# Kernel optimization log

Measured on AMD Instinct MI355X. Metric: run time of the kernel, lower is better.

Reference implementation:

```python
import jax, jax.numpy as jnp
import numpy as np

NUM_USERS = 100000
NUM_ITEMS = 200000
D = 128          # embedding_dim
K = 4            # num interest heads
B = 4096
H = 256          # history length
H1, H2 = 512, 256  # hidden_units


def setup_inputs() -> dict:
    key = jax.random.key(0)
    ks = jax.random.split(key, 10)
    inp = {
        "user_ids": jax.random.randint(ks[0], (B,), 0, NUM_USERS),
        "candidate_items": jax.random.randint(ks[1], (B,), 0, NUM_ITEMS),
        "history_items": jax.random.randint(ks[2], (B, H), 0, NUM_ITEMS),
        "item_table": jax.random.normal(ks[3], (NUM_ITEMS, D), dtype=jnp.float32) * 0.05,
        "Wp": jax.random.normal(ks[4], (D, K), dtype=jnp.float32) * (1.0 / np.sqrt(D)),
        "W1": jax.random.normal(ks[5], (2 * D, H1), dtype=jnp.float32) * (1.0 / np.sqrt(2 * D)),
        "b1": jnp.zeros((H1,), dtype=jnp.float32),
        "W2": jax.random.normal(ks[6], (H1, H2), dtype=jnp.float32) * (1.0 / np.sqrt(H1)),
        "b2": jnp.zeros((H2,), dtype=jnp.float32),
        "W3": jax.random.normal(ks[7], (H2, 1), dtype=jnp.float32) * (1.0 / np.sqrt(H2)),
        "b3": jnp.zeros((1,), dtype=jnp.float32),
    }
    return inp


def reference(user_ids, candidate_items, history_items, item_table, Wp,
              W1, b1, W2, b2, W3, b3):
    # user_ids is unused by the original forward (user_emb never applied)
    item_vecs = item_table[history_items]          # (B, H, D)
    cand_vec = item_table[candidate_items]         # (B, D)

    # per-interest attention scores, softmax over history axis
    scores = jnp.einsum('bhd,dk->bhk', item_vecs, Wp)   # (B, H, K)
    scores = jax.nn.softmax(scores, axis=1)

    # softmax-weighted pooling -> K interest vectors per user
    interest_vectors = jnp.einsum('bhk,bhd->bkd', scores, item_vecs)  # (B, K, D)

    # similarity to candidate, pick best interest (data-dependent gather)
    sim_scores = jnp.einsum('bkd,bd->bk', interest_vectors, cand_vec)  # (B, K)
    best_idx = jnp.argmax(sim_scores, axis=-1)                          # (B,)
    selected = jnp.take_along_axis(
        interest_vectors, best_idx[:, None, None], axis=1)[:, 0, :]    # (B, D)

    # MLP tail: [2D -> 512] ReLU [512 -> 256] ReLU [256 -> 1], sigmoid
    x = jnp.concatenate([selected, cand_vec], axis=-1)  # (B, 2D)
    x = jax.nn.relu(x @ W1 + b1)
    x = jax.nn.relu(x @ W2 + b2)
    out = (x @ W3 + b3)[:, 0]                            # (B,)
    return jax.nn.sigmoid(out)
```

## Files before the change

### kernel.cpp

```cpp
#include <hip/hip_runtime.h>
#include <hip/hip_bf16.h>
#include <math.h>

#define B_SZ   4096
#define H_LEN  256
#define D_DIM  128
#define K_HEADS 4
#define H1_DIM 512
#define H2_DIM 256

#define CH     64
#define NCH    4
#define TPAD   132
#define H1PAD  520

typedef __attribute__((ext_vector_type(8))) short bf16x8;
typedef __attribute__((ext_vector_type(4))) float f32x4;

__global__ __launch_bounds__(256, 4) void interest_kernel(
    const int*   __restrict__ cand_ids,
    const int*   __restrict__ hist,
    const float* __restrict__ table,
    const float* __restrict__ Wp,
    const float* __restrict__ W1,
    const float* __restrict__ W2,
    __hip_bfloat16* __restrict__ W1t,
    __hip_bfloat16* __restrict__ W2t,
    __hip_bfloat16* __restrict__ Xbf)
{
    if (blockIdx.x >= B_SZ) {
        int idx = (blockIdx.x - B_SZ) * 256 + threadIdx.x;
        if (idx < 2 * D_DIM * H1_DIM) {
            int n = idx >> 8, k = idx & 255;
            W1t[idx] = __float2bfloat16(W1[k * H1_DIM + n]);
        } else {
            int j = idx - 2 * D_DIM * H1_DIM;
            int n = j >> 9, k = j & 511;
            W2t[j] = __float2bfloat16(W2[k * H2_DIM + n]);
        }
        return;
    }

    __shared__ float tile[CH * TPAD];
    __shared__ float wpt[K_HEADS * D_DIM];
    __shared__ float exps4[CH * 4];
    __shared__ float candv[D_DIM];
    __shared__ int   rowids[H_LEN];
    __shared__ float lsumW[16];
    __shared__ float simred[4][K_HEADS];
    __shared__ int   bestk;

    const int b    = blockIdx.x;
    const int t    = threadIdx.x;
    const int lane = t & 63, w = t >> 6;
    const int r    = t >> 2, q = t & 3;
    const int d    = t & 127, half = t >> 7;

    if (t < D_DIM) {
        float4 w4 = ((const float4*)Wp)[t];
        wpt[0 * D_DIM + t] = w4.x;
        wpt[1 * D_DIM + t] = w4.y;
        wpt[2 * D_DIM + t] = w4.z;
        wpt[3 * D_DIM + t] = w4.w;
    }
    const int cand = cand_ids[b];
    if (t >= 128 && t < 160) {
        int c = t - 128;
        ((float4*)candv)[c] = ((const float4*)(table + (long long)cand * D_DIM))[c];
    }
    rowids[t] = hist[(long long)b * H_LEN + t];

    float a0 = 0.f, a1 = 0.f, a2 = 0.f, a3 = 0.f;
    float l0 = 0.f, l1 = 0.f, l2 = 0.f, l3 = 0.f;

    for (int c = 0; c < NCH; ++c) {
        __syncthreads();

        const int   row = rowids[(c << 6) + r];
        const float* rp = table + (long long)row * D_DIM + (q << 2);
        float4 v0 = *(const float4*)(rp + 0 * 16);
        float4 v1 = *(const float4*)(rp + 1 * 16);
        float4 v2 = *(const float4*)(rp + 2 * 16);
        float4 v3 = *(const float4*)(rp + 3 * 16);
        float4 v4 = *(const float4*)(rp + 4 * 16);
        float4 v5 = *(const float4*)(rp + 5 * 16);
        float4 v6 = *(const float4*)(rp + 6 * 16);
        float4 v7 = *(const float4*)(rp + 7 * 16);

        float s0 = 0.f, s1 = 0.f, s2 = 0.f, s3 = 0.f;
        float4 va;
        #define DO_J(J, VV)                                                     \
        {   va = VV;                                                            \
            const int cb = (q << 2) + (J << 4);                                 \
            float4 w0 = *(const float4*)(wpt + 0 * D_DIM + cb);                 \
            float4 w1 = *(const float4*)(wpt + 1 * D_DIM + cb);                 \
            float4 w2 = *(const float4*)(wpt + 2 * D_DIM + cb);                 \
            float4 w3 = *(const float4*)(wpt + 3 * D_DIM + cb);                 \
            s0 += va.x * w0.x + va.y * w0.y + va.z * w0.z + va.w * w0.w;        \
            s1 += va.x * w1.x + va.y * w1.y + va.z * w1.z + va.w * w1.w;        \
            s2 += va.x * w2.x + va.y * w2.y + va.z * w2.z + va.w * w2.w;        \
            s3 += va.x * w3.x + va.y * w3.y + va.z * w3.z + va.w * w3.w;        \
            *(float4*)(tile + r * TPAD + cb) = va;                              \
        }
        DO_J(0, v0) DO_J(1, v1) DO_J(2, v2) DO_J(3, v3)
        DO_J(4, v4) DO_J(5, v5) DO_J(6, v6) DO_J(7, v7)
        #undef DO_J

        s0 += __shfl_xor(s0, 1); s0 += __shfl_xor(s0, 2);
        s1 += __shfl_xor(s1, 1); s1 += __shfl_xor(s1, 2);
        s2 += __shfl_xor(s2, 1); s2 += __shfl_xor(s2, 2);
        s3 += __shfl_xor(s3, 1); s3 += __shfl_xor(s3, 2);

        float e0 = expf(s0), e1 = expf(s1), e2 = expf(s2), e3 = expf(s3);
        if (q == 0) ((float4*)exps4)[r] = make_float4(e0, e1, e2, e3);

        float t0 = e0, t1 = e1, t2 = e2, t3 = e3;
        #pragma unroll
        for (int off = 4; off <= 32; off <<= 1) {
            t0 += __shfl_xor(t0, off);
            t1 += __shfl_xor(t1, off);
            t2 += __shfl_xor(t2, off);
            t3 += __shfl_xor(t3, off);
        }
        l0 += t0; l1 += t1; l2 += t2; l3 += t3;

        __syncthreads();

        #pragma unroll 8
        for (int i = 0; i < 32; ++i) {
            int hl = (half << 5) + i;
            float4 e4 = ((const float4*)exps4)[hl];
            float  vv = tile[hl * TPAD + d];
            a0 += e4.x * vv; a1 += e4.y * vv; a2 += e4.z * vv; a3 += e4.w * vv;
        }
    }

    __syncthreads();
    float* partBp = tile;
    float* ivbufp = tile + 512;

    if (half == 1) ((float4*)partBp)[d] = make_float4(a0, a1, a2, a3);
    if (lane == 0) ((float4*)lsumW)[w]  = make_float4(l0, l1, l2, l3);
    __syncthreads();

    float s0 = 0.f, s1 = 0.f, s2 = 0.f, s3 = 0.f;
    if (half == 0) {
        float4 pb = ((const float4*)partBp)[d];
        float4 L0 = ((const float4*)lsumW)[0];
        float4 L1 = ((const float4*)lsumW)[1];
        float4 L2 = ((const float4*)lsumW)[2];
        float4 L3 = ((const float4*)lsumW)[3];
        float i0 = 1.f / (L0.x + L1.x + L2.x + L3.x);
        float i1 = 1.f / (L0.y + L1.y + L2.y + L3.y);
        float i2 = 1.f / (L0.z + L1.z + L2.z + L3.z);
        float i3 = 1.f / (L0.w + L1.w + L2.w + L3.w);
        a0 = (a0 + pb.x) * i0;
        a1 = (a1 + pb.y) * i1;
        a2 = (a2 + pb.z) * i2;
        a3 = (a3 + pb.w) * i3;
        ((float4*)ivbufp)[d] = make_float4(a0, a1, a2, a3);
        float cd = candv[d];
        s0 = a0 * cd; s1 = a1 * cd; s2 = a2 * cd; s3 = a3 * cd;
    }
    #pragma unroll
    for (int off = 32; off >= 1; off >>= 1) {
        s0 += __shfl_xor(s0, off);
        s1 += __shfl_xor(s1, off);
        s2 += __shfl_xor(s2, off);
        s3 += __shfl_xor(s3, off);
    }
    if (lane == 0) {
        simred[w][0] = s0; simred[w][1] = s1;
        simred[w][2] = s2; simred[w][3] = s3;
    }
    __syncthreads();

    if (t == 0) {
        float sim[4];
        #pragma unroll
        for (int k = 0; k < 4; ++k)
            sim[k] = simred[0][k] + simred[1][k] + simred[2][k] + simred[3][k];
        int best = 0;
        #pragma unroll
        for (int k = 1; k < 4; ++k) if (sim[k] > sim[best]) best = k;
        bestk = best;
    }
    __syncthreads();

    __hip_bfloat16* xrow = Xbf + (long long)b * (2 * D_DIM);
    if (t < 128) xrow[t] = __float2bfloat16(ivbufp[t * 4 + bestk]);
    else         xrow[t] = __float2bfloat16(candv[t - 128]);
}

__global__ __launch_bounds__(256) void fused_mlp(
    const __hip_bfloat16* __restrict__ Xbf,
    const __hip_bfloat16* __restrict__ W1t,
    const float* __restrict__ b1,
    const __hip_bfloat16* __restrict__ W2t,
    const float* __restrict__ b2,
    const float* __restrict__ W3,
    const float* __restrict__ b3,
    float* __restrict__ out)
{
    __shared__ __hip_bfloat16 H1s[64 * H1PAD];

    const int t    = threadIdx.x;
    const int wave = t >> 6, lane = t & 63;
    const int lm   = lane & 15, quad = lane >> 4;
    const int mrow = blockIdx.x * 64 + wave * 16;
    const int lrow = wave * 16;

    const __hip_bfloat16* Ap = Xbf + (long long)(mrow + lm) * 256 + quad * 8;
    bf16x8 afr[8];
    #pragma unroll
    for (int j = 0; j < 8; ++j) afr[j] = *(const bf16x8*)(Ap + j * 32);

    #pragma unroll 4
    for (int nt = 0; nt < 32; ++nt) {
        const int n = nt * 16 + lm;
        const __hip_bfloat16* Bp = W1t + (long long)n * 256 + quad * 8;
        f32x4 acc = {0.f, 0.f, 0.f, 0.f};
        #pragma unroll
        for (int j = 0; j < 8; ++j) {
            bf16x8 bfr = *(const bf16x8*)(Bp + j * 32);
            acc = __builtin_amdgcn_mfma_f32_16x16x32_bf16(afr[j], bfr, acc, 0, 0, 0);
        }
        const float bv = b1[n];
        #pragma unroll
        for (int i = 0; i < 4; ++i) {
            float v = fmaxf(acc[i] + bv, 0.f);
            H1s[(lrow + quad * 4 + i) * H1PAD + n] = __float2bfloat16(v);
        }
    }

    bf16x8 hfr[16];
    #pragma unroll
    for (int j = 0; j < 16; ++j)
        hfr[j] = *(const bf16x8*)(&H1s[(lrow + lm) * H1PAD + j * 32 + quad * 8]);

    float hp[4] = {0.f, 0.f, 0.f, 0.f};
    #pragma unroll 2
    for (int nt = 0; nt < 16; ++nt) {
        const int n = nt * 16 + lm;
        const __hip_bfloat16* Bp = W2t + (long long)n * 512 + quad * 8;
        f32x4 acc = {0.f, 0.f, 0.f, 0.f};
        #pragma unroll
        for (int j = 0; j < 16; ++j) {
            bf16x8 bfr = *(const bf16x8*)(Bp + j * 32);
            acc = __builtin_amdgcn_mfma_f32_16x16x32_bf16(hfr[j], bfr, acc, 0, 0, 0);
        }
        const float bv = b2[n], w3v = W3[n];
        #pragma unroll
        for (int i = 0; i < 4; ++i)
            hp[i] += fmaxf(acc[i] + bv, 0.f) * w3v;
    }

    #pragma unroll
    for (int off = 1; off <= 8; off <<= 1) {
        hp[0] += __shfl_xor(hp[0], off);
        hp[1] += __shfl_xor(hp[1], off);
        hp[2] += __shfl_xor(hp[2], off);
        hp[3] += __shfl_xor(hp[3], off);
    }
    if (lm == 0) {
        const float bb = b3[0];
        #pragma unroll
        for (int i = 0; i < 4; ++i) {
            float z = hp[i] + bb;
            out[mrow + quad * 4 + i] = 1.f / (1.f + expf(-z));
        }
    }
}

extern "C" void kernel_launch(void* const* d_in, const int* in_sizes, int n_in,
                              void* d_out, int out_size, void* d_ws, size_t ws_size,
                              hipStream_t stream) {
    const int*   cand  = (const int*)  d_in[1];
    const int*   hist  = (const int*)  d_in[2];
    const float* table = (const float*)d_in[3];
    const float* Wp    = (const float*)d_in[4];
    const float* W1    = (const float*)d_in[5];
    const float* b1    = (const float*)d_in[6];
    const float* W2    = (const float*)d_in[7];
    const float* b2    = (const float*)d_in[8];
    const float* W3    = (const float*)d_in[9];
    const float* b3    = (const float*)d_in[10];
    float* out = (float*)d_out;

    char* p = (char*)d_ws;
    __hip_bfloat16* Xbf = (__hip_bfloat16*)p;  p += (size_t)B_SZ * 2 * D_DIM * 2;
    __hip_bfloat16* W1t = (__hip_bfloat16*)p;  p += (size_t)H1_DIM * 2 * D_DIM * 2;
    __hip_bfloat16* W2t = (__hip_bfloat16*)p;

    interest_kernel<<<B_SZ + 1024, 256, 0, stream>>>(
        cand, hist, table, Wp, W1, W2, W1t, W2t, Xbf);
    fused_mlp<<<B_SZ / 64, 256, 0, stream>>>(Xbf, W1t, b1, W2t, b2, W3, b3, out);
}
```

Measured before the change: 297.1 us.

## Gather history embeddings from a per-call fp16 copy of the item table

When the workspace is large enough, a new kernel converts the whole fp32 item table to fp16 on every call. The interest kernel then gathers history rows at half the bytes, processing 128 rows per chunk with two threads per row and an fp16 shared tile. This targets the bandwidth cost of the random-row gather, but adds a full-table read and write each call and lowers precision. The launch-bounds occupancy hint drops from 4 to 2, and the old fp32 kernel is kept as a fallback when the workspace is too small.

```diff
diff --git a/kernel.cpp b/kernel.cpp
--- a/kernel.cpp
+++ b/kernel.cpp
@@ -8,42 +8,68 @@
 #define K_HEADS 4
 #define H1_DIM 512
 #define H2_DIM 256
+#define NUM_ITEMS 200000
 
 #define CH     64
 #define NCH    4
 #define TPAD   132
 #define H1PAD  520
 
+#define CH2    128
+#define NCH2   2
+#define TP2    136
+
 typedef __attribute__((ext_vector_type(8))) short bf16x8;
 typedef __attribute__((ext_vector_type(4))) float f32x4;
-
-__global__ __launch_bounds__(256, 4) void interest_kernel(
+typedef _Float16 fp16x8 __attribute__((ext_vector_type(8)));
+
+__global__ __launch_bounds__(256) void convert_table(
+    const float* __restrict__ table, _Float16* __restrict__ t16)
+{
+    const int tid = blockIdx.x * 256 + threadIdx.x;
+    float4 a = ((const float4*)table)[tid * 2];
+    float4 b = ((const float4*)table)[tid * 2 + 1];
+    fp16x8 h;
+    h[0] = (_Float16)a.x; h[1] = (_Float16)a.y;
+    h[2] = (_Float16)a.z; h[3] = (_Float16)a.w;
+    h[4] = (_Float16)b.x; h[5] = (_Float16)b.y;
+    h[6] = (_Float16)b.z; h[7] = (_Float16)b.w;
+    ((fp16x8*)t16)[tid] = h;
+}
+
+__device__ __forceinline__ void weight_convert_block(
+    int blk, int t, const float* W1, const float* W2,
+    __hip_bfloat16* W1t, __hip_bfloat16* W2t)
+{
+    int idx = blk * 256 + t;
+    if (idx < 2 * D_DIM * H1_DIM) {
+        int n = idx >> 8, k = idx & 255;
+        W1t[idx] = __float2bfloat16(W1[k * H1_DIM + n]);
+    } else {
+        int j = idx - 2 * D_DIM * H1_DIM;
+        int n = j >> 9, k = j & 511;
+        W2t[j] = __float2bfloat16(W2[k * H2_DIM + n]);
+    }
+}
+
+__global__ __launch_bounds__(256, 2) void interest_kernel_f16(
     const int*   __restrict__ cand_ids,
     const int*   __restrict__ hist,
     const float* __restrict__ table,
+    const _Float16* __restrict__ t16,
     const float* __restrict__ Wp,
-    const float* __restrict__ W1,
-    const float* __restrict__ W2,
-    __hip_bfloat16* __restrict__ W1t,
-    __hip_bfloat16* __restrict__ W2t,
+    const float* __restrict__ W1, const float* __restrict__ W2,
+    __hip_bfloat16* __restrict__ W1t, __hip_bfloat16* __restrict__ W2t,
     __hip_bfloat16* __restrict__ Xbf)
 {
     if (blockIdx.x >= B_SZ) {
-        int idx = (blockIdx.x - B_SZ) * 256 + threadIdx.x;
-        if (idx < 2 * D_DIM * H1_DIM) {
-            int n = idx >> 8, k = idx & 255;
-            W1t[idx] = __float2bfloat16(W1[k * H1_DIM + n]);
-        } else {
-            int j = idx - 2 * D_DIM * H1_DIM;
-            int n = j >> 9, k = j & 511;
-            W2t[j] = __float2bfloat16(W2[k * H2_DIM + n]);
-        }
+        weight_convert_block(blockIdx.x - B_SZ, threadIdx.x, W1, W2, W1t, W2t);
         return;
     }
 
-    __shared__ float tile[CH * TPAD];
+    __shared__ __align__(16) _Float16 tile_h[CH2 * TP2];
     __shared__ float wpt[K_HEADS * D_DIM];
-    __shared__ float exps4[CH * 4];
+    __shared__ float exps4[CH2 * 4];
     __shared__ float candv[D_DIM];
     __shared__ int   rowids[H_LEN];
     __shared__ float lsumW[16];
@@ -53,7 +79,7 @@
     const int b    = blockIdx.x;
     const int t    = threadIdx.x;
     const int lane = t & 63, w = t >> 6;
-    const int r    = t >> 2, q = t & 3;
+    const int rr   = t >> 1, q = t & 1;
     const int d    = t & 127, half = t >> 7;
 
     if (t < D_DIM) {
@@ -73,50 +99,55 @@
     float a0 = 0.f, a1 = 0.f, a2 = 0.f, a3 = 0.f;
     float l0 = 0.f, l1 = 0.f, l2 = 0.f, l3 = 0.f;
 
-    for (int c = 0; c < NCH; ++c) {
+    for (int c = 0; c < NCH2; ++c) {
         __syncthreads();
 
-        const int   row = rowids[(c << 6) + r];
-        const float* rp = table + (long long)row * D_DIM + (q << 2);
-        float4 v0 = *(const float4*)(rp + 0 * 16);
-        float4 v1 = *(const float4*)(rp + 1 * 16);
-        float4 v2 = *(const float4*)(rp + 2 * 16);
-        float4 v3 = *(const float4*)(rp + 3 * 16);
-        float4 v4 = *(const float4*)(rp + 4 * 16);
-        float4 v5 = *(const float4*)(rp + 5 * 16);
-        float4 v6 = *(const float4*)(rp + 6 * 16);
-        float4 v7 = *(const float4*)(rp + 7 * 16);
+        const int row = rowids[(c << 7) + rr];
+        const fp16x8* rp = (const fp16x8*)(t16 + (long long)row * D_DIM + (q << 6));
+        fp16x8 v0 = rp[0], v1 = rp[1], v2 = rp[2], v3 = rp[3];
+        fp16x8 v4 = rp[4], v5 = rp[5], v6 = rp[6], v7 = rp[7];
 
         float s0 = 0.f, s1 = 0.f, s2 = 0.f, s3 = 0.f;
-        float4 va;
         #define DO_J(J, VV)                                                     \
-        {   va = VV;                                                            \
-            const int cb = (q << 2) + (J << 4);                                 \
-            float4 w0 = *(const float4*)(wpt + 0 * D_DIM + cb);                 \
-            float4 w1 = *(const float4*)(wpt + 1 * D_DIM + cb);                 \
-            float4 w2 = *(const float4*)(wpt + 2 * D_DIM + cb);                 \
-            float4 w3 = *(const float4*)(wpt + 3 * D_DIM + cb);                 \
-            s0 += va.x * w0.x + va.y * w0.y + va.z * w0.z + va.w * w0.w;        \
-            s1 += va.x * w1.x + va.y * w1.y + va.z * w1.z + va.w * w1.w;        \
-            s2 += va.x * w2.x + va.y * w2.y + va.z * w2.z + va.w * w2.w;        \
-            s3 += va.x * w3.x + va.y * w3.y + va.z * w3.z + va.w * w3.w;        \
-            *(float4*)(tile + r * TPAD + cb) = va;                              \
+        {   fp16x8 va = VV;                                                     \
+            const int db = (q << 6) + (J << 3);                                 \
+            float ax = (float)va[0], ay = (float)va[1];                         \
+            float az = (float)va[2], aw = (float)va[3];                         \
+            float bx = (float)va[4], by = (float)va[5];                         \
+            float bz = (float)va[6], bw = (float)va[7];                         \
+            float4 w0l = *(const float4*)(wpt + 0 * D_DIM + db);                \
+            float4 w0h = *(const float4*)(wpt + 0 * D_DIM + db + 4);            \
+            float4 w1l = *(const float4*)(wpt + 1 * D_DIM + db);                \
+            float4 w1h = *(const float4*)(wpt + 1 * D_DIM + db + 4);            \
+            float4 w2l = *(const float4*)(wpt + 2 * D_DIM + db);                \
+            float4 w2h = *(const float4*)(wpt + 2 * D_DIM + db + 4);            \
+            float4 w3l = *(const float4*)(wpt + 3 * D_DIM + db);                \
+            float4 w3h = *(const float4*)(wpt + 3 * D_DIM + db + 4);            \
+            s0 += ax*w0l.x + ay*w0l.y + az*w0l.z + aw*w0l.w                     \
+                + bx*w0h.x + by*w0h.y + bz*w0h.z + bw*w0h.w;                    \
+            s1 += ax*w1l.x + ay*w1l.y + az*w1l.z + aw*w1l.w                     \
+                + bx*w1h.x + by*w1h.y + bz*w1h.z + bw*w1h.w;                    \
+            s2 += ax*w2l.x + ay*w2l.y + az*w2l.z + aw*w2l.w                     \
+                + bx*w2h.x + by*w2h.y + bz*w2h.z + bw*w2h.w;                    \
+            s3 += ax*w3l.x + ay*w3l.y + az*w3l.z + aw*w3l.w                     \
+                + bx*w3h.x + by*w3h.y + bz*w3h.z + bw*w3h.w;                    \
+            *(fp16x8*)(tile_h + rr * TP2 + db) = va;                            \
         }
         DO_J(0, v0) DO_J(1, v1) DO_J(2, v2) DO_J(3, v3)
         DO_J(4, v4) DO_J(5, v5) DO_J(6, v6) DO_J(7, v7)
         #undef DO_J
 
-        s0 += __shfl_xor(s0, 1); s0 += __shfl_xor(s0, 2);
-        s1 += __shfl_xor(s1, 1); s1 += __shfl_xor(s1, 2);
-        s2 += __shfl_xor(s2, 1); s2 += __shfl_xor(s2, 2);
-        s3 += __shfl_xor(s3, 1); s3 += __shfl_xor(s3, 2);
+        s0 += __shfl_xor(s0, 1);
+        s1 += __shfl_xor(s1, 1);
+        s2 += __shfl_xor(s2, 1);
+        s3 += __shfl_xor(s3, 1);
 
         float e0 = expf(s0), e1 = expf(s1), e2 = expf(s2), e3 = expf(s3);
-        if (q == 0) ((float4*)exps4)[r] = make_float4(e0, e1, e2, e3);
+        if (q == 0) ((float4*)exps4)[rr] = make_float4(e0, e1, e2, e3);
 
         float t0 = e0, t1 = e1, t2 = e2, t3 = e3;
         #pragma unroll
-        for (int off = 4; off <= 32; off <<= 1) {
+        for (int off = 2; off <= 32; off <<= 1) {
             t0 += __shfl_xor(t0, off);
             t1 += __shfl_xor(t1, off);
             t2 += __shfl_xor(t2, off);
@@ -127,17 +158,17 @@
         __syncthreads();
 
         #pragma unroll 8
-        for (int i = 0; i < 32; ++i) {
-            int hl = (half << 5) + i;
+        for (int i = 0; i < 64; ++i) {
+            int hl = (half << 6) + i;
             float4 e4 = ((const float4*)exps4)[hl];
-            float  vv = tile[hl * TPAD + d];
+            float  vv = (float)tile_h[hl * TP2 + d];
             a0 += e4.x * vv; a1 += e4.y * vv; a2 += e4.z * vv; a3 += e4.w * vv;
         }
     }
 
     __syncthreads();
-    float* partBp = tile;
-    float* ivbufp = tile + 512;
+    float* partBp = (float*)tile_h;
+    float* ivbufp = (float*)tile_h + 512;
 
     if (half == 1) ((float4*)partBp)[d] = make_float4(a0, a1, a2, a3);
     if (lane == 0) ((float4*)lsumW)[w]  = make_float4(l0, l1, l2, l3);
@@ -192,6 +223,171 @@
     else         xrow[t] = __float2bfloat16(candv[t - 128]);
 }
 
+__global__ __launch_bounds__(256, 4) void interest_kernel_f32(
+    const int*   __restrict__ cand_ids,
+    const int*   __restrict__ hist,
+    const float* __restrict__ table,
+    const float* __restrict__ Wp,
+    const float* __restrict__ W1, const float* __restrict__ W2,
+    __hip_bfloat16* __restrict__ W1t, __hip_bfloat16* __restrict__ W2t,
+    __hip_bfloat16* __restrict__ Xbf)
+{
+    if (blockIdx.x >= B_SZ) {
+        weight_convert_block(blockIdx.x - B_SZ, threadIdx.x, W1, W2, W1t, W2t);
+        return;
+    }
+
+    __shared__ float tile[CH * TPAD];
+    __shared__ float wpt[K_HEADS * D_DIM];
+    __shared__ float exps4[CH * 4];
+    __shared__ float candv[D_DIM];
+    __shared__ int   rowids[H_LEN];
+    __shared__ float lsumW[16];
+    __shared__ float simred[4][K_HEADS];
+    __shared__ int   bestk;
+
+    const int b    = blockIdx.x;
+    const int t    = threadIdx.x;
+    const int lane = t & 63, w = t >> 6;
+    const int r    = t >> 2, q = t & 3;
+    const int d    = t & 127, half = t >> 7;
+
+    if (t < D_DIM) {
+        float4 w4 = ((const float4*)Wp)[t];
+        wpt[0 * D_DIM + t] = w4.x;
+        wpt[1 * D_DIM + t] = w4.y;
+        wpt[2 * D_DIM + t] = w4.z;
+        wpt[3 * D_DIM + t] = w4.w;
+    }
+    const int cand = cand_ids[b];
+    if (t >= 128 && t < 160) {
+        int c = t - 128;
+        ((float4*)candv)[c] = ((const float4*)(table + (long long)cand * D_DIM))[c];
+    }
+    rowids[t] = hist[(long long)b * H_LEN + t];
+
+    float a0 = 0.f, a1 = 0.f, a2 = 0.f, a3 = 0.f;
+    float l0 = 0.f, l1 = 0.f, l2 = 0.f, l3 = 0.f;
+
+    for (int c = 0; c < NCH; ++c) {
+        __syncthreads();
+
+        const int   row = rowids[(c << 6) + r];
+        const float* rp = table + (long long)row * D_DIM + (q << 2);
+        float4 v0 = *(const float4*)(rp + 0 * 16);
+        float4 v1 = *(const float4*)(rp + 1 * 16);
+        float4 v2 = *(const float4*)(rp + 2 * 16);
+        float4 v3 = *(const float4*)(rp + 3 * 16);
+        float4 v4 = *(const float4*)(rp + 4 * 16);
+        float4 v5 = *(const float4*)(rp + 5 * 16);
+        float4 v6 = *(const float4*)(rp + 6 * 16);
+        float4 v7 = *(const float4*)(rp + 7 * 16);
+
+        float s0 = 0.f, s1 = 0.f, s2 = 0.f, s3 = 0.f;
+        float4 va;
+        #define DO_J(J, VV)                                                     \
+        {   va = VV;                                                            \
+            const int cb = (q << 2) + (J << 4);                                 \
+            float4 w0 = *(const float4*)(wpt + 0 * D_DIM + cb);                 \
+            float4 w1 = *(const float4*)(wpt + 1 * D_DIM + cb);                 \
+            float4 w2 = *(const float4*)(wpt + 2 * D_DIM + cb);                 \
+            float4 w3 = *(const float4*)(wpt + 3 * D_DIM + cb);                 \
+            s0 += va.x * w0.x + va.y * w0.y + va.z * w0.z + va.w * w0.w;        \
+            s1 += va.x * w1.x + va.y * w1.y + va.z * w1.z + va.w * w1.w;        \
+            s2 += va.x * w2.x + va.y * w2.y + va.z * w2.z + va.w * w2.w;        \
+            s3 += va.x * w3.x + va.y * w3.y + va.z * w3.z + va.w * w3.w;        \
+            *(float4*)(tile + r * TPAD + cb) = va;                              \
+        }
+        DO_J(0, v0) DO_J(1, v1) DO_J(2, v2) DO_J(3, v3)
+        DO_J(4, v4) DO_J(5, v5) DO_J(6, v6) DO_J(7, v7)
+        #undef DO_J
+
+        s0 += __shfl_xor(s0, 1); s0 += __shfl_xor(s0, 2);
+        s1 += __shfl_xor(s1, 1); s1 += __shfl_xor(s1, 2);
+        s2 += __shfl_xor(s2, 1); s2 += __shfl_xor(s2, 2);
+        s3 += __shfl_xor(s3, 1); s3 += __shfl_xor(s3, 2);
+
+        float e0 = expf(s0), e1 = expf(s1), e2 = expf(s2), e3 = expf(s3);
+        if (q == 0) ((float4*)exps4)[r] = make_float4(e0, e1, e2, e3);
+
+        float t0 = e0, t1 = e1, t2 = e2, t3 = e3;
+        #pragma unroll
+        for (int off = 4; off <= 32; off <<= 1) {
+            t0 += __shfl_xor(t0, off);
+            t1 += __shfl_xor(t1, off);
+            t2 += __shfl_xor(t2, off);
+            t3 += __shfl_xor(t3, off);
+        }
+        l0 += t0; l1 += t1; l2 += t2; l3 += t3;
+
+        __syncthreads();
+
+        #pragma unroll 8
+        for (int i = 0; i < 32; ++i) {
+            int hl = (half << 5) + i;
+            float4 e4 = ((const float4*)exps4)[hl];
+            float  vv = tile[hl * TPAD + d];
+            a0 += e4.x * vv; a1 += e4.y * vv; a2 += e4.z * vv; a3 += e4.w * vv;
+        }
+    }
+
+    __syncthreads();
+    float* partBp = tile;
+    float* ivbufp = tile + 512;
+
+    if (half == 1) ((float4*)partBp)[d] = make_float4(a0, a1, a2, a3);
+    if (lane == 0) ((float4*)lsumW)[w]  = make_float4(l0, l1, l2, l3);
+    __syncthreads();
+
+    float s0 = 0.f, s1 = 0.f, s2 = 0.f, s3 = 0.f;
+    if (half == 0) {
+        float4 pb = ((const float4*)partBp)[d];
+        float4 L0 = ((const float4*)lsumW)[0];
+        float4 L1 = ((const float4*)lsumW)[1];
+        float4 L2 = ((const float4*)lsumW)[2];
+        float4 L3 = ((const float4*)lsumW)[3];
+        float i0 = 1.f / (L0.x + L1.x + L2.x + L3.x);
+        float i1 = 1.f / (L0.y + L1.y + L2.y + L3.y);
+        float i2 = 1.f / (L0.z + L1.z + L2.z + L3.z);
+        float i3 = 1.f / (L0.w + L1.w + L2.w + L3.w);
+        a0 = (a0 + pb.x) * i0;
+        a1 = (a1 + pb.y) * i1;
+        a2 = (a2 + pb.z) * i2;
+        a3 = (a3 + pb.w) * i3;
+        ((float4*)ivbufp)[d] = make_float4(a0, a1, a2, a3);
+        float cd = candv[d];
+        s0 = a0 * cd; s1 = a1 * cd; s2 = a2 * cd; s3 = a3 * cd;
+    }
+    #pragma unroll
+    for (int off = 32; off >= 1; off >>= 1) {
+        s0 += __shfl_xor(s0, off);
+        s1 += __shfl_xor(s1, off);
+        s2 += __shfl_xor(s2, off);
+        s3 += __shfl_xor(s3, off);
+    }
+    if (lane == 0) {
+        simred[w][0] = s0; simred[w][1] = s1;
+        simred[w][2] = s2; simred[w][3] = s3;
+    }
+    __syncthreads();
+
+    if (t == 0) {
+        float sim[4];
+        #pragma unroll
+        for (int k = 0; k < 4; ++k)
+            sim[k] = simred[0][k] + simred[1][k] + simred[2][k] + simred[3][k];
+        int best = 0;
+        #pragma unroll
+        for (int k = 1; k < 4; ++k) if (sim[k] > sim[best]) best = k;
+        bestk = best;
+    }
+    __syncthreads();
+
+    __hip_bfloat16* xrow = Xbf + (long long)b * (2 * D_DIM);
+    if (t < 128) xrow[t] = __float2bfloat16(ivbufp[t * 4 + bestk]);
+    else         xrow[t] = __float2bfloat16(candv[t - 128]);
+}
+
 __global__ __launch_bounds__(256) void fused_mlp(
     const __hip_bfloat16* __restrict__ Xbf,
     const __hip_bfloat16* __restrict__ W1t,
@@ -287,12 +483,26 @@
     const float* b3    = (const float*)d_in[10];
     float* out = (float*)d_out;
 
+    const size_t t16_bytes = (size_t)NUM_ITEMS * D_DIM * 2;
+    const size_t xbf_bytes = (size_t)B_SZ * 2 * D_DIM * 2;
+    const size_t w1t_bytes = (size_t)H1_DIM * 2 * D_DIM * 2;
+    const size_t w2t_bytes = (size_t)H2_DIM * H1_DIM * 2;
+    const bool   use16 = ws_size >= t16_bytes + xbf_bytes + w1t_bytes + w2t_bytes;
+
     char* p = (char*)d_ws;
-    __hip_bfloat16* Xbf = (__hip_bfloat16*)p;  p += (size_t)B_SZ * 2 * D_DIM * 2;
-    __hip_bfloat16* W1t = (__hip_bfloat16*)p;  p += (size_t)H1_DIM * 2 * D_DIM * 2;
+    _Float16* t16 = nullptr;
+    if (use16) { t16 = (_Float16*)p; p += t16_bytes; }
+    __hip_bfloat16* Xbf = (__hip_bfloat16*)p;  p += xbf_bytes;
+    __hip_bfloat16* W1t = (__hip_bfloat16*)p;  p += w1t_bytes;
     __hip_bfloat16* W2t = (__hip_bfloat16*)p;
 
-    interest_kernel<<<B_SZ + 1024, 256, 0, stream>>>(
-        cand, hist, table, Wp, W1, W2, W1t, W2t, Xbf);
+    if (use16) {
+        convert_table<<<(NUM_ITEMS * D_DIM / 8) / 256, 256, 0, stream>>>(table, t16);
+        interest_kernel_f16<<<B_SZ + 1024, 256, 0, stream>>>(
+            cand, hist, table, t16, Wp, W1, W2, W1t, W2t, Xbf);
+    } else {
+        interest_kernel_f32<<<B_SZ + 1024, 256, 0, stream>>>(
+            cand, hist, table, Wp, W1, W2, W1t, W2t, Xbf);
+    }
     fused_mlp<<<B_SZ / 64, 256, 0, stream>>>(Xbf, W1t, b1, W2t, b2, W3, b3, out);
 }
```

Result: slower. 319.3 us (+7.5%).
